# Kernel tuning notes

Measured on AMD Instinct MI355X. Metric: run time of the kernel, lower is better.

Reference implementation:

```python
import jax, jax.numpy as jnp
import numpy as np

B, N, D = 16, 1024, 16  # graphs, nodes, embedding_dim


def setup_inputs() -> dict:
    key = jax.random.key(0)
    ks = jax.random.split(key, 13)
    s = 0.05  # small weight scale to keep exp(alpha) well-behaved
    return {
        "X": jax.random.normal(ks[0], (B, N, D), dtype=jnp.float32),
        "init_param": jax.random.normal(ks[1], (2,), dtype=jnp.float32) * s,
        "Wq": jax.random.normal(ks[2], (D - 1, D, D), dtype=jnp.float32) * s,
        "bq": jax.random.normal(ks[3], (D - 1, D), dtype=jnp.float32) * s,
        "Wk": jax.random.normal(ks[4], (D - 1, D, D), dtype=jnp.float32) * s,
        "bk": jax.random.normal(ks[5], (D - 1, D), dtype=jnp.float32) * s,
        "Wv": jax.random.normal(ks[6], (D - 1, D, D), dtype=jnp.float32) * s,
        "bv": jax.random.normal(ks[7], (D - 1, D), dtype=jnp.float32) * s,
        "Wo": jax.random.normal(ks[8], (D - 1, D, D), dtype=jnp.float32) * s,
        "bo": jax.random.normal(ks[9], (D - 1, D), dtype=jnp.float32) * s,
        "Wf": jax.random.normal(ks[10], (D - 1, 2, D), dtype=jnp.float32) * s,
        "bf": jax.random.normal(ks[11], (D - 1, 2), dtype=jnp.float32) * s,
    }


def reference(X, init_param, Wq, bq, Wk, bk, Wv, bv, Wo, bo, Wf, bf):
    b, n, d = X.shape
    dt = X.dtype
    Zs = []
    logdet = jnp.zeros((b, n), dt)
    for i in range(d):
        if i == 0:
            mu, alpha = init_param[0], init_param[1]
        else:
            l = i - 1
            Xi = X[:, :, :i]  # [B,N,i] growing ragged slice
            Q = Xi @ Wq[l, :i, :i].T + bq[l, :i]
            K = Xi @ Wk[l, :i, :i].T + bk[l, :i]
            V = Xi @ Wv[l, :i, :i].T + bv[l, :i]
            # SAB/MAB: softmax(QK^T / sqrt(dim_V=i)); num_heads=1
            A = jax.nn.softmax(
                jnp.einsum("bnd,bmd->bnm", Q, K) / jnp.sqrt(jnp.asarray(i, dt)),
                axis=-1,
            )  # [B,N,N]
            O = Q + jnp.einsum("bnm,bmd->bnd", A, V)
            O = O + jax.nn.relu(O @ Wo[l, :i, :i].T + bo[l, :i])
            out = O @ Wf[l, :, :i].T + bf[l]  # [B,N,2]
            mu, alpha = out[..., 0], out[..., 1]
        Zs.append((X[:, :, i] - mu) / jnp.exp(alpha))
        logdet = logdet - alpha
    Z = jnp.stack(Zs, axis=-1)
    return Z, logdet
```

## Files before the change

kernel.cpp:

```cpp
#include <hip/hip_runtime.h>
#include <math.h>

#define Bb 16
#define Nn 1024
#define Dd 16
#define NL 15

typedef __attribute__((ext_vector_type(8))) short short8;
typedef __attribute__((ext_vector_type(16))) float f32x16;
typedef __attribute__((ext_vector_type(4))) unsigned uint4v;

#if __has_builtin(__builtin_amdgcn_exp2f)
#define EXP2(x) __builtin_amdgcn_exp2f(x)
#else
#define EXP2(x) exp2f(x)
#endif

#define VSTR 1044
#define V_OFF 32768
#define RS_OFF 69632
#define ONES_OFF 73728
#define LDS_TOTAL 75776

__device__ __forceinline__ unsigned pack2bf(float a, float b) {
    unsigned ua = __float_as_uint(a) + 0x8000u;
    unsigned ub = __float_as_uint(b) + 0x8000u;
    return (ua >> 16) | (ub & 0xffff0000u);
}
__device__ __forceinline__ unsigned short bf1(float a) {
    return (unsigned short)((__float_as_uint(a) + 0x8000u) >> 16);
}

__device__ __forceinline__ unsigned expperm(float x, float y) {
    unsigned ex = __float_as_uint(EXP2(x));
    unsigned ey = __float_as_uint(EXP2(y));
#if __has_builtin(__builtin_amdgcn_perm)
    return __builtin_amdgcn_perm(ey, ex, 0x07060302);
#else
    return (ex >> 16) | (ey & 0xffff0000u);
#endif
}

__device__ __forceinline__ void project(const float* __restrict__ xrow,
                                        const float* __restrict__ W,
                                        const float* __restrict__ bias,
                                        int i, float* __restrict__ q) {
#pragma unroll
    for (int r = 0; r < 16; r++) q[r] = 0.f;
    for (int c = 0; c < i; c++) {
        float xc = xrow[c];
#pragma unroll
        for (int r = 0; r < 16; r++) q[r] = fmaf(xc, W[r * 16 + c], q[r]);
    }
#pragma unroll
    for (int r = 0; r < 16; r++) q[r] = (r < i) ? (q[r] + bias[r]) : 0.f;
}

__device__ __forceinline__ void load_row16(const float* __restrict__ p, float* __restrict__ x) {
    const float4* xp = (const float4*)p;
    float4 a = xp[0], b = xp[1], c = xp[2], d = xp[3];
    x[0]=a.x; x[1]=a.y; x[2]=a.z; x[3]=a.w;
    x[4]=b.x; x[5]=b.y; x[6]=b.z; x[7]=b.w;
    x[8]=c.x; x[9]=c.y; x[10]=c.z; x[11]=c.w;
    x[12]=d.x; x[13]=d.y; x[14]=d.z; x[15]=d.w;
}

__device__ __forceinline__ short8 ldv(const unsigned short* __restrict__ p) {
    uint2 a = *(const uint2*)p;
    uint2 b = *(const uint2*)(p + 8);
    uint4v v = {a.x, a.y, b.x, b.y};
    return __builtin_bit_cast(short8, v);
}

__global__ void gf_init(const float* __restrict__ X, const float* __restrict__ ip,
                        float* __restrict__ out) {
    int idx = blockIdx.x * blockDim.x + threadIdx.x;
    if (idx >= Bb * Nn) return;
    float mu = ip[0], alpha = ip[1];
    float x0 = X[(size_t)idx * Dd];
    out[(size_t)idx * Dd] = (x0 - mu) * __expf(-alpha);
    out[(size_t)Bb * Nn * Dd + idx] = -alpha;
}

__launch_bounds__(1024, 4)
__global__ void gf_fused(const float* __restrict__ X,
                         const float* __restrict__ Wq, const float* __restrict__ bq,
                         const float* __restrict__ Wk, const float* __restrict__ bk,
                         const float* __restrict__ Wv, const float* __restrict__ bv,
                         const float* __restrict__ Wo, const float* __restrict__ bo,
                         const float* __restrict__ Wf, const float* __restrict__ bf,
                         float* __restrict__ out) {
    extern __shared__ char smem[];
    const int l = blockIdx.x, b = blockIdx.y, i = l + 1;
    const int t = threadIdx.x;
    const int wid = t >> 6, lane = t & 63;
    const int q31 = lane & 31, h = lane >> 5;
    const float qscale = 1.4426950408889634f * rsqrtf((float)i);

    unsigned short* Ksh  = (unsigned short*)smem;
    unsigned short* Vsh  = (unsigned short*)(smem + V_OFF);
    unsigned short* Ones = (unsigned short*)(smem + ONES_OFF);

    const float* Xb  = X  + (size_t)b * Nn * Dd;
    const float* wq  = Wq + l * 256;  const float* bql = bq + l * 16;
    const float* wk  = Wk + l * 256;  const float* bkl = bk + l * 16;
    const float* wvp = Wv + l * 256;  const float* bvl = bv + l * 16;
    const float* wo  = Wo + l * 256;  const float* bol = bo + l * 16;
    const float* wf  = Wf + l * 32;   const float* bfl = bf + l * 2;

    unsigned qu[8];
    {
        float xr[16]; load_row16(Xb + (size_t)t * Dd, xr);
        float tmp[16];
        unsigned u[8];

        project(xr, wk, bkl, i, tmp);
#pragma unroll
        for (int r = 0; r < 8; r++) u[r] = pack2bf(tmp[2*r], tmp[2*r+1]);
        {
            uint4* kd = (uint4*)(Ksh + t * 16);
            kd[0] = make_uint4(u[0], u[1], u[2], u[3]);
            kd[1] = make_uint4(u[4], u[5], u[6], u[7]);
        }

        project(xr, wvp, bvl, i, tmp);
#pragma unroll
        for (int d = 0; d < 16; d++) Vsh[d * VSTR + t] = bf1(tmp[d]);

        Ones[t] = 0x3F80;

        project(xr, wq, bql, i, tmp);
#pragma unroll
        for (int r = 0; r < 8; r++) qu[r] = pack2bf(tmp[2*r] * qscale, tmp[2*r+1] * qscale);
    }
    __syncthreads();

    short8 qf0, qf1;
    {
        unsigned d0[4], d1[4];
#pragma unroll
        for (int j = 0; j < 4; j++) {
            unsigned lo = __shfl(qu[j], q31);
            unsigned hi = __shfl(qu[4 + j], q31);
            d0[j] = h ? hi : lo;
            lo = __shfl(qu[j], 32 + q31);
            hi = __shfl(qu[4 + j], 32 + q31);
            d1[j] = h ? hi : lo;
        }
        uint4v v0 = {d0[0], d0[1], d0[2], d0[3]};
        uint4v v1 = {d1[0], d1[1], d1[2], d1[3]};
        qf0 = __builtin_bit_cast(short8, v0);
        qf1 = __builtin_bit_cast(short8, v1);
    }

    f32x16 zf16 = {};
    f32x16 D0 = {}, D1 = {};

    const unsigned short* Kp = Ksh + (size_t)q31 * 16 + h * 8;
    const unsigned short* Vp = ((q31 < 16) ? (Vsh + (size_t)q31 * VSTR) : Ones) + 4 * h;

    short8 kf  = *(const short8*)Kp;
    short8 vc0 = ldv(Vp);
    short8 vc1 = ldv(Vp + 16);

    for (int kb = 0; kb < Nn; kb += 32) {
        const int kn = (kb + 32) & (Nn - 1);
        short8 kfn = *(const short8*)(Kp + (size_t)kn * 16);
        short8 vn0 = ldv(Vp + kn);
        short8 vn1 = ldv(Vp + kn + 16);

        f32x16 s0 = __builtin_amdgcn_mfma_f32_32x32x16_bf16(kf, qf0, zf16, 0, 0, 0);
        f32x16 s1 = __builtin_amdgcn_mfma_f32_32x32x16_bf16(kf, qf1, zf16, 0, 0, 0);
        kf = kfn;

        {
            uint4v a0 = {expperm(s0[0], s0[1]), expperm(s0[2], s0[3]),
                         expperm(s0[4], s0[5]), expperm(s0[6], s0[7])};
            D0 = __builtin_amdgcn_mfma_f32_32x32x16_bf16(
                     __builtin_bit_cast(short8, a0), vc0, D0, 0, 0, 0);
            uint4v a1 = {expperm(s1[0], s1[1]), expperm(s1[2], s1[3]),
                         expperm(s1[4], s1[5]), expperm(s1[6], s1[7])};
            D1 = __builtin_amdgcn_mfma_f32_32x32x16_bf16(
                     __builtin_bit_cast(short8, a1), vc0, D1, 0, 0, 0);
        }
        {
            uint4v a0 = {expperm(s0[8], s0[9]),  expperm(s0[10], s0[11]),
                         expperm(s0[12], s0[13]), expperm(s0[14], s0[15])};
            D0 = __builtin_amdgcn_mfma_f32_32x32x16_bf16(
                     __builtin_bit_cast(short8, a0), vc1, D0, 0, 0, 0);
            uint4v a1 = {expperm(s1[8], s1[9]),  expperm(s1[10], s1[11]),
                         expperm(s1[12], s1[13]), expperm(s1[14], s1[15])};
            D1 = __builtin_amdgcn_mfma_f32_32x32x16_bf16(
                     __builtin_bit_cast(short8, a1), vc1, D1, 0, 0, 0);
        }
        vc0 = vn0; vc1 = vn1;
    }

    __syncthreads();

    float* Ow = (float*)smem + wid * (64 * 17);
    if (q31 < 16) {
#pragma unroll
        for (int r = 0; r < 16; r++) {
            int m = (r & 3) + 8 * (r >> 2) + 4 * h;
            Ow[m * 17 + q31]        = D0[r];
            Ow[(m + 32) * 17 + q31] = D1[r];
        }
    }
    float* Rw = (float*)(smem + RS_OFF) + wid * 64;
    if (q31 == 16) {
#pragma unroll
        for (int r = 0; r < 16; r++) {
            int m = (r & 3) + 8 * (r >> 2) + 4 * h;
            Rw[m]      = D0[r];
            Rw[32 + m] = D1[r];
        }
    }

    {
        float xr[16]; load_row16(Xb + (size_t)t * Dd, xr);
        float q[16];  project(xr, wq, bql, i, q);
        const float* orow = (const float*)smem + wid * (64 * 17) + lane * 17;
        const float  inv  = 1.f / Rw[lane];

        float a[16];
#pragma unroll
        for (int c = 0; c < 16; c++) a[c] = q[c] + orow[c] * inv;

        float tt[16];
#pragma unroll
        for (int r = 0; r < 16; r++) {
            float acc = bol[r];
#pragma unroll
            for (int c = 0; c < 16; c++) acc = fmaf(a[c], wo[r * 16 + c], acc);
            tt[r] = fmaxf(acc, 0.f);
        }
#pragma unroll
        for (int r = 0; r < 16; r++) a[r] += (r < i) ? tt[r] : 0.f;

        float mu = bfl[0], al = bfl[1];
#pragma unroll
        for (int c = 0; c < 16; c++) {
            mu = fmaf(a[c], wf[c], mu);
            al = fmaf(a[c], wf[16 + c], al);
        }
        out[((size_t)(b * Nn + t)) * Dd + i] = (xr[i] - mu) * __expf(-al);
        atomicAdd(out + (size_t)Bb * Nn * Dd + b * Nn + t, -al);
    }
}

__launch_bounds__(512, 2)
__global__ void gf_layer_fb(const float* __restrict__ X,
                            const float* __restrict__ Wq, const float* __restrict__ bq,
                            const float* __restrict__ Wk, const float* __restrict__ bk,
                            const float* __restrict__ Wv, const float* __restrict__ bv,
                            const float* __restrict__ Wo, const float* __restrict__ bo,
                            const float* __restrict__ Wf, const float* __restrict__ bf,
                            float* __restrict__ out) {
    const int l = blockIdx.x, b = blockIdx.y, i = l + 1, t = threadIdx.x;
    const float rscale = rsqrtf((float)i);
    __shared__ float Ksh[512 * 16];
    __shared__ float Vsh[512 * 16];
    const float* Xb = X + (size_t)b * Nn * Dd;
    const float* wq = Wq + l * 256; const float* wk = Wk + l * 256;
    const float* wv = Wv + l * 256; const float* wo = Wo + l * 256;
    const float* wf = Wf + l * 32;
    const float* bql = bq + l * 16; const float* bkl = bk + l * 16;
    const float* bvl = bv + l * 16; const float* bol = bo + l * 16;
    const float* bfl = bf + l * 2;
    const int n0 = t, n1 = t + 512;
    float q0[16], q1[16], xi0, xi1;
    {
        float xr[16];
        load_row16(Xb + (size_t)n0 * Dd, xr); xi0 = xr[i]; project(xr, wq, bql, i, q0);
        load_row16(Xb + (size_t)n1 * Dd, xr); xi1 = xr[i]; project(xr, wq, bql, i, q1);
    }
    float o0[16], o1[16];
#pragma unroll
    for (int c = 0; c < 16; c++) { o0[c] = 0.f; o1[c] = 0.f; }
    float ls0 = 0.f, ls1 = 0.f;
    for (int ch = 0; ch < 2; ch++) {
        float kr[16], vr[16];
        {
            float kx[16];
            load_row16(Xb + (size_t)(ch * 512 + t) * Dd, kx);
            project(kx, wk, bkl, i, kr);
            project(kx, wv, bvl, i, vr);
        }
        __syncthreads();
#pragma unroll
        for (int j = 0; j < 4; j++) {
            ((float4*)&Ksh[t * 16])[j] = ((float4*)kr)[j];
            ((float4*)&Vsh[t * 16])[j] = ((float4*)vr)[j];
        }
        __syncthreads();
        for (int k = 0; k < 512; k++) {
            float kk[16], vv[16];
#pragma unroll
            for (int j = 0; j < 4; j++) ((float4*)kk)[j] = ((const float4*)&Ksh[k * 16])[j];
            float s0 = 0.f, s1 = 0.f;
#pragma unroll
            for (int c = 0; c < 16; c++) { s0 = fmaf(q0[c], kk[c], s0); s1 = fmaf(q1[c], kk[c], s1); }
            float p0 = __expf(s0 * rscale), p1 = __expf(s1 * rscale);
            ls0 += p0; ls1 += p1;
#pragma unroll
            for (int j = 0; j < 4; j++) ((float4*)vv)[j] = ((const float4*)&Vsh[k * 16])[j];
#pragma unroll
            for (int c = 0; c < 16; c++) { o0[c] = fmaf(p0, vv[c], o0[c]); o1[c] = fmaf(p1, vv[c], o1[c]); }
        }
        __syncthreads();
    }
    float* logdet = out + (size_t)Bb * Nn * Dd;
#pragma unroll
    for (int rowsel = 0; rowsel < 2; rowsel++) {
        const float* qr = rowsel ? q1 : q0; const float* orr = rowsel ? o1 : o0;
        float lsum = rowsel ? ls1 : ls0; float xin = rowsel ? xi1 : xi0;
        int n = rowsel ? n1 : n0;
        float a[16]; float inv = 1.f / lsum;
#pragma unroll
        for (int c = 0; c < 16; c++) a[c] = qr[c] + orr[c] * inv;
        float tt[16];
#pragma unroll
        for (int r = 0; r < 16; r++) {
            float acc = bol[r];
#pragma unroll
            for (int c = 0; c < 16; c++) acc = fmaf(a[c], wo[r * 16 + c], acc);
            tt[r] = fmaxf(acc, 0.f);
        }
#pragma unroll
        for (int r = 0; r < 16; r++) a[r] += (r < i) ? tt[r] : 0.f;
        float mu = bfl[0], al = bfl[1];
#pragma unroll
        for (int c = 0; c < 16; c++) { mu = fmaf(a[c], wf[c], mu); al = fmaf(a[c], wf[16 + c], al); }
        out[((size_t)(b * Nn + n)) * Dd + i] = (xin - mu) * __expf(-al);
        atomicAdd(logdet + b * Nn + n, -al);
    }
}

extern "C" void kernel_launch(void* const* d_in, const int* in_sizes, int n_in,
                              void* d_out, int out_size, void* d_ws, size_t ws_size,
                              hipStream_t stream) {
    const float* X  = (const float*)d_in[0];
    const float* ip = (const float*)d_in[1];
    const float* Wq = (const float*)d_in[2];
    const float* bq = (const float*)d_in[3];
    const float* Wk = (const float*)d_in[4];
    const float* bk = (const float*)d_in[5];
    const float* Wv = (const float*)d_in[6];
    const float* bv = (const float*)d_in[7];
    const float* Wo = (const float*)d_in[8];
    const float* bo = (const float*)d_in[9];
    const float* Wf = (const float*)d_in[10];
    const float* bf = (const float*)d_in[11];
    float* out = (float*)d_out;

    gf_init<<<(Bb * Nn + 255) / 256, 256, 0, stream>>>(X, ip, out);

    hipError_t e = hipFuncSetAttribute((const void*)gf_fused,
                                       hipFuncAttributeMaxDynamicSharedMemorySize,
                                       LDS_TOTAL);
    if (e == hipSuccess) {
        gf_fused<<<dim3(NL, Bb), 1024, LDS_TOTAL, stream>>>(
            X, Wq, bq, Wk, bk, Wv, bv, Wo, bo, Wf, bf, out);
    } else {
        gf_layer_fb<<<dim3(NL, Bb), 512, 0, stream>>>(
            X, Wq, bq, Wk, bk, Wv, bv, Wo, bo, Wf, bf, out);
    }
}
```

Measured before the change: 140.7 us.

## Split query rows across two blocks per layer-graph to double grid parallelism

The fused attention kernel now launches a third grid dimension of 2, so each block handles 512 query rows (32 per wave) instead of 1024 (64 per wave), while every block still projects the full K and V into LDS. The grid grows from 240 to 480 blocks, which spreads work across more CUs. The cost is that the K/V projection and LDS fill are done twice. The V-fragment register prefetch is dropped, LDS usage shrinks, and the launch-bounds occupancy hint rises from 4 to 8, which may force register spilling.

```diff
diff --git a/kernel.cpp b/kernel.cpp
--- a/kernel.cpp
+++ b/kernel.cpp
@@ -18,9 +18,9 @@
 
 #define VSTR 1044
 #define V_OFF 32768
-#define RS_OFF 69632
-#define ONES_OFF 73728
-#define LDS_TOTAL 75776
+#define ONES_OFF 66176
+#define RS_OFF 36864
+#define LDS_TOTAL 68224
 
 __device__ __forceinline__ unsigned pack2bf(float a, float b) {
     unsigned ua = __float_as_uint(a) + 0x8000u;
@@ -82,7 +82,7 @@
     out[(size_t)Bb * Nn * Dd + idx] = -alpha;
 }
 
-__launch_bounds__(1024, 4)
+__launch_bounds__(1024, 8)
 __global__ void gf_fused(const float* __restrict__ X,
                          const float* __restrict__ Wq, const float* __restrict__ bq,
                          const float* __restrict__ Wk, const float* __restrict__ bk,
@@ -91,10 +91,11 @@
                          const float* __restrict__ Wf, const float* __restrict__ bf,
                          float* __restrict__ out) {
     extern __shared__ char smem[];
-    const int l = blockIdx.x, b = blockIdx.y, i = l + 1;
+    const int l = blockIdx.x, b = blockIdx.y, z = blockIdx.z, i = l + 1;
     const int t = threadIdx.x;
     const int wid = t >> 6, lane = t & 63;
     const int q31 = lane & 31, h = lane >> 5;
+    const int qbase = z * 512 + wid * 32;
     const float qscale = 1.4426950408889634f * rsqrtf((float)i);
 
     unsigned short* Ksh  = (unsigned short*)smem;
@@ -129,98 +130,80 @@
 
         Ones[t] = 0x3F80;
 
-        project(xr, wq, bql, i, tmp);
+        float xq[16]; load_row16(Xb + (size_t)(qbase + q31) * Dd, xq);
+        project(xq, wq, bql, i, tmp);
 #pragma unroll
         for (int r = 0; r < 8; r++) qu[r] = pack2bf(tmp[2*r] * qscale, tmp[2*r+1] * qscale);
     }
     __syncthreads();
 
-    short8 qf0, qf1;
+    short8 qf;
     {
-        unsigned d0[4], d1[4];
+        unsigned d0[4];
 #pragma unroll
         for (int j = 0; j < 4; j++) {
             unsigned lo = __shfl(qu[j], q31);
             unsigned hi = __shfl(qu[4 + j], q31);
             d0[j] = h ? hi : lo;
-            lo = __shfl(qu[j], 32 + q31);
-            hi = __shfl(qu[4 + j], 32 + q31);
-            d1[j] = h ? hi : lo;
         }
         uint4v v0 = {d0[0], d0[1], d0[2], d0[3]};
-        uint4v v1 = {d1[0], d1[1], d1[2], d1[3]};
-        qf0 = __builtin_bit_cast(short8, v0);
-        qf1 = __builtin_bit_cast(short8, v1);
+        qf = __builtin_bit_cast(short8, v0);
     }
 
     f32x16 zf16 = {};
-    f32x16 D0 = {}, D1 = {};
+    f32x16 D0 = {};
 
     const unsigned short* Kp = Ksh + (size_t)q31 * 16 + h * 8;
     const unsigned short* Vp = ((q31 < 16) ? (Vsh + (size_t)q31 * VSTR) : Ones) + 4 * h;
 
-    short8 kf  = *(const short8*)Kp;
-    short8 vc0 = ldv(Vp);
-    short8 vc1 = ldv(Vp + 16);
+    short8 kf = *(const short8*)Kp;
 
     for (int kb = 0; kb < Nn; kb += 32) {
         const int kn = (kb + 32) & (Nn - 1);
-        short8 kfn = *(const short8*)(Kp + (size_t)kn * 16);
-        short8 vn0 = ldv(Vp + kn);
-        short8 vn1 = ldv(Vp + kn + 16);
-
-        f32x16 s0 = __builtin_amdgcn_mfma_f32_32x32x16_bf16(kf, qf0, zf16, 0, 0, 0);
-        f32x16 s1 = __builtin_amdgcn_mfma_f32_32x32x16_bf16(kf, qf1, zf16, 0, 0, 0);
-        kf = kfn;
+        short8 vc0 = ldv(Vp + kb);
+        short8 vc1 = ldv(Vp + kb + 16);
+
+        f32x16 s0 = __builtin_amdgcn_mfma_f32_32x32x16_bf16(kf, qf, zf16, 0, 0, 0);
+        kf = *(const short8*)(Kp + (size_t)kn * 16);
 
         {
             uint4v a0 = {expperm(s0[0], s0[1]), expperm(s0[2], s0[3]),
                          expperm(s0[4], s0[5]), expperm(s0[6], s0[7])};
             D0 = __builtin_amdgcn_mfma_f32_32x32x16_bf16(
                      __builtin_bit_cast(short8, a0), vc0, D0, 0, 0, 0);
-            uint4v a1 = {expperm(s1[0], s1[1]), expperm(s1[2], s1[3]),
-                         expperm(s1[4], s1[5]), expperm(s1[6], s1[7])};
-            D1 = __builtin_amdgcn_mfma_f32_32x32x16_bf16(
-                     __builtin_bit_cast(short8, a1), vc0, D1, 0, 0, 0);
         }
         {
-            uint4v a0 = {expperm(s0[8], s0[9]),  expperm(s0[10], s0[11]),
+            uint4v a1 = {expperm(s0[8], s0[9]),  expperm(s0[10], s0[11]),
                          expperm(s0[12], s0[13]), expperm(s0[14], s0[15])};
             D0 = __builtin_amdgcn_mfma_f32_32x32x16_bf16(
-                     __builtin_bit_cast(short8, a0), vc1, D0, 0, 0, 0);
-            uint4v a1 = {expperm(s1[8], s1[9]),  expperm(s1[10], s1[11]),
-                         expperm(s1[12], s1[13]), expperm(s1[14], s1[15])};
-            D1 = __builtin_amdgcn_mfma_f32_32x32x16_bf16(
-                     __builtin_bit_cast(short8, a1), vc1, D1, 0, 0, 0);
-        }
-        vc0 = vn0; vc1 = vn1;
+                     __builtin_bit_cast(short8, a1), vc1, D0, 0, 0, 0);
+        }
     }
 
     __syncthreads();
 
-    float* Ow = (float*)smem + wid * (64 * 17);
+    float* Ow = (float*)smem + wid * (32 * 17);
     if (q31 < 16) {
 #pragma unroll
         for (int r = 0; r < 16; r++) {
             int m = (r & 3) + 8 * (r >> 2) + 4 * h;
-            Ow[m * 17 + q31]        = D0[r];
-            Ow[(m + 32) * 17 + q31] = D1[r];
-        }
-    }
-    float* Rw = (float*)(smem + RS_OFF) + wid * 64;
+            Ow[m * 17 + q31] = D0[r];
+        }
+    }
+    float* Rw = (float*)(smem + RS_OFF) + wid * 32;
     if (q31 == 16) {
 #pragma unroll
         for (int r = 0; r < 16; r++) {
             int m = (r & 3) + 8 * (r >> 2) + 4 * h;
-            Rw[m]      = D0[r];
-            Rw[32 + m] = D1[r];
-        }
-    }
-
-    {
-        float xr[16]; load_row16(Xb + (size_t)t * Dd, xr);
+            Rw[m] = D0[r];
+        }
+    }
+
+    if (lane < 32) {
+        const int n = qbase + lane;
+        float xr[16]; load_row16(Xb + (size_t)n * Dd, xr);
         float q[16];  project(xr, wq, bql, i, q);
-        const float* orow = (const float*)smem + wid * (64 * 17) + lane * 17;
+        const float* orow = (const float*)smem + wid * (32 * 17) + lane * 17;
         const float  inv  = 1.f / Rw[lane];
 
         float a[16];
@@ -244,8 +227,8 @@
             mu = fmaf(a[c], wf[c], mu);
             al = fmaf(a[c], wf[16 + c], al);
         }
-        out[((size_t)(b * Nn + t)) * Dd + i] = (xr[i] - mu) * __expf(-al);
-        atomicAdd(out + (size_t)Bb * Nn * Dd + b * Nn + t, -al);
+        out[((size_t)(b * Nn + n)) * Dd + i] = (xr[i] - mu) * __expf(-al);
+        atomicAdd(out + (size_t)Bb * Nn * Dd + b * Nn + n, -al);
     }
 }
 
@@ -360,7 +343,7 @@
                                        hipFuncAttributeMaxDynamicSharedMemorySize,
                                        LDS_TOTAL);
     if (e == hipSuccess) {
-        gf_fused<<<dim3(NL, Bb), 1024, LDS_TOTAL, stream>>>(
+        gf_fused<<<dim3(NL, Bb, 2), 1024, LDS_TOTAL, stream>>>(
             X, Wq, bq, Wk, bk, Wv, bv, Wo, bo, Wf, bf, out);
     } else {
         gf_layer_fb<<<dim3(NL, Bb), 512, 0, stream>>>(
```

New measurement: 169.0 us. 1.2x slower.

## Permute V layout in LDS for single 128-bit loads and reuse packed Q

Applied to the files above, without the earlier changes.

V is now stored transposed with a within-16 permutation of token positions, so each lane can fetch its 8 bf16 V values with one 128-bit LDS load instead of two 64-bit loads. The row stride and LDS offsets shrink to match. The epilogue no longer reloads X and recomputes the Q projection; it rebuilds Q from the bf16-packed, pre-scaled registers, which lowers Q precision in the residual path. The permutation must line up with the MFMA K ordering, which adds some correctness risk.

```diff
diff --git a/kernel.cpp b/kernel.cpp
--- a/kernel.cpp
+++ b/kernel.cpp
@@ -16,11 +16,11 @@
 #define EXP2(x) exp2f(x)
 #endif
 
-#define VSTR 1044
+#define VSTR 1040
 #define V_OFF 32768
+#define ONES_OFF 66048
 #define RS_OFF 69632
-#define ONES_OFF 73728
-#define LDS_TOTAL 75776
+#define LDS_TOTAL 73728
 
 __device__ __forceinline__ unsigned pack2bf(float a, float b) {
     unsigned ua = __float_as_uint(a) + 0x8000u;
@@ -41,6 +41,10 @@
 #endif
 }
 
+__device__ __forceinline__ int vperm(int m) {
+    return (m & 3) + ((m & 8) >> 1) + ((m & 4) << 1);
+}
+
 __device__ __forceinline__ void project(const float* __restrict__ xrow,
                                         const float* __restrict__ W,
                                         const float* __restrict__ bias,
@@ -63,13 +67,6 @@
     x[4]=b.x; x[5]=b.y; x[6]=b.z; x[7]=b.w;
     x[8]=c.x; x[9]=c.y; x[10]=c.z; x[11]=c.w;
     x[12]=d.x; x[13]=d.y; x[14]=d.z; x[15]=d.w;
-}
-
-__device__ __forceinline__ short8 ldv(const unsigned short* __restrict__ p) {
-    uint2 a = *(const uint2*)p;
-    uint2 b = *(const uint2*)(p + 8);
-    uint4v v = {a.x, a.y, b.x, b.y};
-    return __builtin_bit_cast(short8, v);
 }
 
 __global__ void gf_init(const float* __restrict__ X, const float* __restrict__ ip,
@@ -112,20 +109,23 @@
     {
         float xr[16]; load_row16(Xb + (size_t)t * Dd, xr);
         float tmp[16];
-        unsigned u[8];
 
         project(xr, wk, bkl, i, tmp);
-#pragma unroll
-        for (int r = 0; r < 8; r++) u[r] = pack2bf(tmp[2*r], tmp[2*r+1]);
-        {
+        {
+            unsigned u[8];
+#pragma unroll
+            for (int r = 0; r < 8; r++) u[r] = pack2bf(tmp[2*r], tmp[2*r+1]);
             uint4* kd = (uint4*)(Ksh + t * 16);
             kd[0] = make_uint4(u[0], u[1], u[2], u[3]);
             kd[1] = make_uint4(u[4], u[5], u[6], u[7]);
         }
 
         project(xr, wvp, bvl, i, tmp);
-#pragma unroll
-        for (int d = 0; d < 16; d++) Vsh[d * VSTR + t] = bf1(tmp[d]);
+        {
+            unsigned short* vcol = Vsh + (t & ~15) + vperm(t & 15);
+#pragma unroll
+            for (int d = 0; d < 16; d++) vcol[d * VSTR] = bf1(tmp[d]);
+        }
 
         Ones[t] = 0x3F80;
 
@@ -157,17 +157,17 @@
     f32x16 D0 = {}, D1 = {};
 
     const unsigned short* Kp = Ksh + (size_t)q31 * 16 + h * 8;
-    const unsigned short* Vp = ((q31 < 16) ? (Vsh + (size_t)q31 * VSTR) : Ones) + 4 * h;
+    const unsigned short* Vp = ((q31 < 16) ? (Vsh + (size_t)q31 * VSTR) : Ones) + 8 * h;
 
     short8 kf  = *(const short8*)Kp;
-    short8 vc0 = ldv(Vp);
-    short8 vc1 = ldv(Vp + 16);
+    short8 vc0 = *(const short8*)(Vp);
+    short8 vc1 = *(const short8*)(Vp + 16);
 
     for (int kb = 0; kb < Nn; kb += 32) {
         const int kn = (kb + 32) & (Nn - 1);
         short8 kfn = *(const short8*)(Kp + (size_t)kn * 16);
-        short8 vn0 = ldv(Vp + kn);
-        short8 vn1 = ldv(Vp + kn + 16);
+        short8 vn0 = *(const short8*)(Vp + kn);
+        short8 vn1 = *(const short8*)(Vp + kn + 16);
 
         f32x16 s0 = __builtin_amdgcn_mfma_f32_32x32x16_bf16(kf, qf0, zf16, 0, 0, 0);
         f32x16 s1 = __builtin_amdgcn_mfma_f32_32x32x16_bf16(kf, qf1, zf16, 0, 0, 0);
@@ -218,14 +218,19 @@
     }
 
     {
-        float xr[16]; load_row16(Xb + (size_t)t * Dd, xr);
-        float q[16];  project(xr, wq, bql, i, q);
+        const float invq = 0.6931471805599453f * sqrtf((float)i);
+
+        float a[16];
+#pragma unroll
+        for (int r = 0; r < 8; r++) {
+            a[2*r]     = __uint_as_float(qu[r] << 16) * invq;
+            a[2*r + 1] = __uint_as_float(qu[r] & 0xffff0000u) * invq;
+        }
+
         const float* orow = (const float*)smem + wid * (64 * 17) + lane * 17;
         const float  inv  = 1.f / Rw[lane];
-
-        float a[16];
-#pragma unroll
-        for (int c = 0; c < 16; c++) a[c] = q[c] + orow[c] * inv;
+#pragma unroll
+        for (int c = 0; c < 16; c++) a[c] += orow[c] * inv;
 
         float tt[16];
 #pragma unroll
@@ -244,7 +249,8 @@
             mu = fmaf(a[c], wf[c], mu);
             al = fmaf(a[c], wf[16 + c], al);
         }
-        out[((size_t)(b * Nn + t)) * Dd + i] = (xr[i] - mu) * __expf(-al);
+        const float xi = Xb[(size_t)t * Dd + i];
+        out[((size_t)(b * Nn + t)) * Dd + i] = (xi - mu) * __expf(-al);
         atomicAdd(out + (size_t)Bb * Nn * Dd + b * Nn + t, -al);
     }
 }
```

Result: faster. 133.4 us (-5.2%).
